# Performance work log

Measured on AMD Instinct MI355X. Metric: run time of the kernel, lower is better.

## Reference

```python
import jax, jax.numpy as jnp
import numpy as np

B, T = 256, 25
PRE = 2048   # resnet feature dim
D = 256      # fc_early_dim = cell_size = in_size = hybrid_in_size
K = 4        # num_atts
NC = 2       # num_classes


def setup_inputs() -> dict:
    key = jax.random.key(0)
    ks = jax.random.split(key, 20)
    def p(k, *s):
        return jax.random.normal(k, s, jnp.float32) * 0.02
    z = lambda *s: jnp.zeros(s, jnp.float32)
    return {
        "x_visual": jax.random.normal(ks[0], (B, T, PRE), jnp.float32),
        "x_tactile": jax.random.normal(ks[1], (B, T, PRE), jnp.float32),
        "fc0_w": p(ks[2], PRE, D), "fc0_b": z(D),
        "fc1_w": p(ks[3], PRE, D), "fc1_b": z(D),
        # LSTHM_V: W(x) + U(h) + V(z), gates packed as [f,i,o,ch]
        "lv_W": p(ks[4], D, 4 * D), "lv_U": p(ks[5], D, 4 * D), "lv_V": p(ks[6], D, 4 * D), "lv_b": z(4 * D),
        # LSTHM_T
        "lt_W": p(ks[7], D, 4 * D), "lt_U": p(ks[8], D, 4 * D), "lt_V": p(ks[9], D, 4 * D), "lt_b": z(4 * D),
        # MAB: attention over concat hidden (2D) producing K attentions
        "att_w": p(ks[10], 2 * D, K * 2 * D), "att_b": z(K * 2 * D),
        "red_v_w": p(ks[11], K * D, D), "red_v_b": z(D),
        "red_t_w": p(ks[12], K * D, D), "red_t_b": z(D),
        "mab_out_w": p(ks[13], 2 * D, D), "mab_out_b": z(D),
        "late0_w": p(ks[14], 2 * D, D), "late0_b": z(D),
        "late1_w": p(ks[15], D, NC), "late1_b": z(NC),
    }


def _lsthm(x, c, h, zz, W, U, V, b):
    s = x @ W + h @ U + zz @ V + b            # [B, 4D]
    f = jax.nn.sigmoid(s[:, :D])
    i = jax.nn.sigmoid(s[:, D:2 * D])
    o = jax.nn.sigmoid(s[:, 2 * D:3 * D])
    ch = jnp.tanh(s[:, 3 * D:])
    c_new = f * c + i * ch
    return c_new, jnp.tanh(c_new) * o


def reference(x_visual, x_tactile, fc0_w, fc0_b, fc1_w, fc1_b,
              lv_W, lv_U, lv_V, lv_b, lt_W, lt_U, lt_V, lt_b,
              att_w, att_b, red_v_w, red_v_b, red_t_w, red_t_b,
              mab_out_w, mab_out_b, late0_w, late0_b, late1_w, late1_b):
    xv = x_visual @ fc0_w + fc0_b             # [B, T, D]
    xt = x_tactile @ fc1_w + fc1_b            # [B, T, D]

    def mab(h_v, h_t):
        h = jnp.concatenate([h_v, h_t], -1)   # [B, 2D]
        att = jax.nn.softmax(h @ att_w + att_b, axis=-1)       # [B, K*2D]
        attd = att.reshape(-1, K, 2 * D) * h[:, None, :]        # K attended copies
        v = attd[:, :, :D].reshape(-1, K * D)
        t = attd[:, :, D:].reshape(-1, K * D)
        rv = jax.nn.relu(v @ red_v_w + red_v_b)
        rt = jax.nn.relu(t @ red_t_w + red_t_b)
        return jnp.concatenate([rv, rt], -1) @ mab_out_w + mab_out_b  # [B, D]

    def step(carry, xs):
        c_v, h_v, c_t, h_t, zz = carry
        xvi, xti = xs
        c_v, h_v = _lsthm(xvi, c_v, h_v, zz, lv_W, lv_U, lv_V, lv_b)
        c_t, h_t = _lsthm(xti, c_t, h_t, zz, lt_W, lt_U, lt_V, lt_b)
        zz = mab(h_v, h_t)
        return (c_v, h_v, c_t, h_t, zz), None

    zeros = jnp.zeros((x_visual.shape[0], D), jnp.float32)
    init = (zeros, zeros, zeros, zeros, zeros)
    (c_v, h_v, c_t, h_t, zz), _ = jax.lax.scan(
        step, init, (jnp.swapaxes(xv, 0, 1), jnp.swapaxes(xt, 0, 1)))
    x = jnp.concatenate([h_v, h_t], -1) @ late0_w + late0_b
    return x @ late1_w + late1_b              # dropout is identity in eval
```

## Files before the change

### kernel.cpp

```cpp
#include <hip/hip_runtime.h>

typedef unsigned short u16;
typedef unsigned int u32;
typedef unsigned long long u64;
using bfrag = __attribute__((ext_vector_type(8))) short;
using facc  = __attribute__((ext_vector_type(4))) float;

#define DEV __device__ __forceinline__
#define AGT __HIP_MEMORY_SCOPE_AGENT

static constexpr size_t o_xv  = 0;
static constexpr size_t o_xt  = 3276800;
static constexpr size_t o_Wxv = 6553600;
static constexpr size_t o_Wxt = 19660800;
static constexpr size_t o_f0T = 32768000;
static constexpr size_t o_f1T = 33816576;
static constexpr size_t o_UV  = 34865152;
static constexpr size_t o_Wpv = 36962304;
static constexpr size_t o_Wpt = 37486592;
static constexpr size_t o_bpv = 38010880;
static constexpr size_t o_bpt = 38014976;
static constexpr size_t o_attT= 38019072;
static constexpr size_t o_redT= 40116224;
static constexpr size_t o_mabT= 41164800;
static constexpr size_t o_FW  = 41426944;
static constexpr size_t o_fb  = 41431040;
static constexpr size_t o_eh  = 41431296;
static constexpr size_t o_rvt = 42479872;
static constexpr size_t o_ps  = 42742016;
static constexpr size_t o_hv0 = 42807552;
static constexpr size_t o_hv1 = 42938624;
static constexpr size_t o_ht0 = 43069696;
static constexpr size_t o_ht1 = 43200768;
static constexpr size_t o_zz  = 43331840;
static constexpr size_t o_bar = 43462912;
static constexpr size_t o_end = 43463936;

DEV u16 f2bf(float f) {
    u32 u = __float_as_uint(f);
    u32 r = (u + 0x7FFFu + ((u >> 16) & 1u)) >> 16;
    return (u16)r;
}
DEV float bf2f(u16 h) { return __uint_as_float(((u32)h) << 16); }
DEV u32 pk2(float a, float b) { return (u32)f2bf(a) | ((u32)f2bf(b) << 16); }
DEV float sigm(float x) { return 1.0f / (1.0f + __expf(-x)); }
DEV float tanh2(float x) { return 2.0f * sigm(2.0f * x) - 1.0f; }
DEV facc mfma16(bfrag a, bfrag b, facc c) {
    return __builtin_amdgcn_mfma_f32_16x16x32_bf16(a, b, c, 0, 0, 0);
}

DEV u64 ld64c(const void* p) { return __hip_atomic_load((u64*)p, __ATOMIC_RELAXED, AGT); }
DEV uint4 ld_c16(const void* p) {
    u64 a = ld64c(p), b = ld64c((const char*)p + 8);
    uint4 r; r.x = (u32)a; r.y = (u32)(a >> 32); r.z = (u32)b; r.w = (u32)(b >> 32); return r;
}
DEV float ldf32c(const float* p) {
    return __uint_as_float(__hip_atomic_load((u32*)p, __ATOMIC_RELAXED, AGT));
}
DEV void sw32(void* p, u32 v) { (void)__hip_atomic_exchange((u32*)p, v, __ATOMIC_RELAXED, AGT); }
DEV void sw64(void* p, u64 v) { (void)__hip_atomic_exchange((u64*)p, v, __ATOMIC_RELAXED, AGT); }
DEV void sw128(void* p, uint4 v) {
    sw64(p, ((u64)v.y << 32) | v.x);
    sw64((char*)p + 8, ((u64)v.w << 32) | v.z);
}
DEV void swf32(float* p, float v) { sw32(p, __float_as_uint(v)); }

DEV void gbar(u32* bar, int bid, u32 k) {
    asm volatile("s_waitcnt vmcnt(0)" ::: "memory");
    __syncthreads();
    if (threadIdx.x == 0) {
        __builtin_amdgcn_fence(__ATOMIC_RELEASE, "agent");
        u32 old = __hip_atomic_fetch_add(&bar[(bid & 7) * 16], 1u, __ATOMIC_RELAXED, AGT);
        if (old == k * 32u - 1u)
            __hip_atomic_fetch_add(&bar[128], 1u, __ATOMIC_RELAXED, AGT);
        while (__hip_atomic_load(&bar[128], __ATOMIC_RELAXED, AGT) < k * 8u)
            __builtin_amdgcn_s_sleep(2);
    }
    __syncthreads();
}


DEV void prep_T(const float* __restrict__ src, u16* dst, int lgK, int N, int nb, int bl, int tid) {
    int pairs = ((1 << lgK) * N) >> 1;
    int kmask = (1 << lgK) - 1;
    for (int idx = bl * 256 + tid; idx < pairs; idx += nb * 256) {
        int i = idx * 2;
        int n = i >> lgK, k = i & kmask;
        sw32(dst + i, pk2(src[(size_t)k * N + n], src[(size_t)(k + 1) * N + n]));
    }
}

DEV void prep_UV(const float* U, const float* V, u16* dst, int nb, int bl, int tid) {
    for (int idx = bl * 256 + tid; idx < 262144; idx += nb * 256) {
        int i = idx * 2;
        int p = i >> 9, k = i & 511;
        int j = p >> 2, g = p & 3;
        float v0 = (k < 256) ? U[(size_t)k * 1024 + g * 256 + j] : V[(size_t)(k - 256) * 1024 + g * 256 + j];
        float v1 = (k + 1 < 256) ? U[(size_t)(k + 1) * 1024 + g * 256 + j] : V[(size_t)(k - 255) * 1024 + g * 256 + j];
        sw32(dst + i, pk2(v0, v1));
    }
}

DEV void prep_W(const float* W, const float* bsrc, u16* dst, float* bpk, int nb, int bl, int tid) {
    for (int idx = bl * 256 + tid; idx < 131072; idx += nb * 256) {
        int i = idx * 2;
        int p = i >> 8, k = i & 255;
        int j = p >> 2, g = p & 3;
        sw32(dst + i, pk2(W[(size_t)k * 1024 + g * 256 + j], W[(size_t)(k + 1) * 1024 + g * 256 + j]));
        if (k == 0) swf32(&bpk[p], bsrc[g * 256 + j]);
    }
}

DEV void prep_FW(const float* l0w, const float* l0b, const float* l1w, const float* l1b,
                 float* FW, float* fb, int tid) {
    for (int idx = tid; idx < 1024; idx += 256) {
        int k = idx >> 1, c = idx & 1;
        float a = 0.f;
        for (int j = 0; j < 256; ++j) a += l0w[k * 256 + j] * l1w[j * 2 + c];
        swf32(&FW[idx], a);
    }
    if (tid < 2) {
        float a = l1b[tid];
        for (int j = 0; j < 256; ++j) a += l0b[j] * l1w[j * 2 + tid];
        swf32(&fb[tid], a);
    }
}

struct KP { const float* in[26]; char* ws; float* out; };


__global__ __launch_bounds__(256) void marn_all(KP P) {
    __shared__ __align__(16) unsigned char SM[31744];
    int tid = threadIdx.x, b = blockIdx.x;
    int w = tid >> 6, l = tid & 63, lm = l & 15, kh = l >> 4;
    u32 bk = 0;
    char* ws = P.ws;

    u16* f0T = (u16*)(ws + o_f0T);
    u16* f1T = (u16*)(ws + o_f1T);
    u16* attT = (u16*)(ws + o_attT);
    u16* redT = (u16*)(ws + o_redT);
    u16* mabT = (u16*)(ws + o_mabT);
    u16* UVpk = (u16*)(ws + o_UV);
    u16* Wpv = (u16*)(ws + o_Wpv);
    u16* Wpt = (u16*)(ws + o_Wpt);
    float* bpv = (float*)(ws + o_bpv);
    float* bpt = (float*)(ws + o_bpt);
    float* FW = (float*)(ws + o_FW);
    float* fb = (float*)(ws + o_fb);
    u16* xv = (u16*)(ws + o_xv);
    u16* xt = (u16*)(ws + o_xt);
    u16* Wxv = (u16*)(ws + o_Wxv);
    u16* Wxt = (u16*)(ws + o_Wxt);
    u16* eh = (u16*)(ws + o_eh);
    u16* rvt = (u16*)(ws + o_rvt);
    u16* hv0 = (u16*)(ws + o_hv0);
    u16* hv1 = (u16*)(ws + o_hv1);
    u16* ht0 = (u16*)(ws + o_ht0);
    u16* ht1 = (u16*)(ws + o_ht1);
    u16* zz = (u16*)(ws + o_zz);
    float* psum = (float*)(ws + o_ps);
    u32* bar = (u32*)(ws + o_bar);
    const float* attb = P.in[15];
    const float* rvb = P.in[17];
    const float* rtb = P.in[19];
    const float* mob = P.in[21];

    if      (b < 32)  prep_T(P.in[2], f0T, 11, 256, 32, b, tid);
    else if (b < 64)  prep_T(P.in[4], f1T, 11, 256, 32, b - 32, tid);
    else if (b < 128) prep_T(P.in[14], attT, 9, 2048, 64, b - 64, tid);
    else if (b < 144) prep_T(P.in[16], redT, 10, 256, 16, b - 128, tid);
    else if (b < 160) prep_T(P.in[18], redT + 256 * 1024, 10, 256, 16, b - 144, tid);
    else if (b < 168) prep_T(P.in[20], mabT, 9, 256, 8, b - 160, tid);
    else if (b < 200) prep_UV(P.in[7], P.in[8], UVpk, 32, b - 168, tid);
    else if (b < 232) prep_UV(P.in[11], P.in[12], UVpk + 1024 * 512, 32, b - 200, tid);
    else if (b < 244) prep_W(P.in[6], P.in[9], Wpv, bpv, 12, b - 232, tid);
    else if (b < 255) prep_W(P.in[10], P.in[13], Wpt, bpt, 11, b - 244, tid);
    else              prep_FW(P.in[22], P.in[23], P.in[24], P.in[25], FW, fb, tid);
    gbar(bar, b, ++bk);

    {
        u16* Al = (u16*)SM;
        u16* Bl = (u16*)(SM + 9216);
        u16* Lt = (u16*)SM;
        for (int u = b; u < 400; u += 256) {
            int zs = u & 1, ny = (u >> 1) & 1, mx = u >> 2;
            const float* A = zs ? P.in[1] : P.in[0];
            const u16* BT = zs ? f1T : f0T;
            const float* bias = zs ? P.in[5] : P.in[3];
            u16* C = zs ? xt : xv;
            int m0 = mx * 64, n0 = ny * 128;
            int arow = tid >> 2, aseg = tid & 3;
            int brow = tid >> 1, bseg = tid & 1;
            facc acc[8];
#pragma unroll
            for (int i = 0; i < 8; ++i) acc[i] = (facc){0.f, 0.f, 0.f, 0.f};
            for (int c = 0; c < 32; ++c) {
                float4 av[4];
#pragma unroll
                for (int uu = 0; uu < 4; ++uu)
                    av[uu] = *(const float4*)&A[(size_t)(m0 + arow) * 2048 + c * 64 + aseg * 16 + uu * 4];
                uint4 bv[4];
#pragma unroll
                for (int uu = 0; uu < 4; ++uu)
                    bv[uu] = *(const uint4*)&BT[(size_t)(n0 + brow) * 2048 + c * 64 + bseg * 32 + uu * 8];
                __syncthreads();
                u32 pk[8];
#pragma unroll
                for (int uu = 0; uu < 4; ++uu) {
                    pk[2 * uu] = pk2(av[uu].x, av[uu].y);
                    pk[2 * uu + 1] = pk2(av[uu].z, av[uu].w);
                }
                *(uint4*)&Al[arow * 72 + aseg * 16] = make_uint4(pk[0], pk[1], pk[2], pk[3]);
                *(uint4*)&Al[arow * 72 + aseg * 16 + 8] = make_uint4(pk[4], pk[5], pk[6], pk[7]);
#pragma unroll
                for (int uu = 0; uu < 4; ++uu)
                    *(uint4*)&Bl[brow * 72 + bseg * 32 + uu * 8] = bv[uu];
                __syncthreads();
#pragma unroll
                for (int ks = 0; ks < 2; ++ks) {
                    bfrag a = *(const bfrag*)&Al[(16 * w + lm) * 72 + ks * 32 + kh * 8];
#pragma unroll
                    for (int tt = 0; tt < 8; ++tt) {
                        bfrag bb = *(const bfrag*)&Bl[(tt * 16 + lm) * 72 + ks * 32 + kh * 8];
                        acc[tt] = mfma16(a, bb, acc[tt]);
                    }
                }
            }
            __syncthreads();
#pragma unroll
            for (int tt = 0; tt < 8; ++tt)
#pragma unroll
                for (int j = 0; j < 4; ++j)
                    Lt[(16 * w + 4 * kh + j) * 128 + tt * 16 + lm] = f2bf(acc[tt][j] + bias[n0 + tt * 16 + lm]);
            __syncthreads();
            {
                int mloc = tid >> 2, seg = tid & 3;
                const uint4* lp = (const uint4*)&Lt[mloc * 128 + seg * 32];
                sw128(&C[(size_t)(m0 + mloc) * 256 + n0 + seg * 32], lp[0]);
                sw128(&C[(size_t)(m0 + mloc) * 256 + n0 + seg * 32 + 8], lp[1]);
                sw128(&C[(size_t)(m0 + mloc) * 256 + n0 + seg * 32 + 16], lp[2]);
                sw128(&C[(size_t)(m0 + mloc) * 256 + n0 + seg * 32 + 24], lp[3]);
            }
            __syncthreads();
        }
    }
    gbar(bar, b, ++bk);

    {
        u16* Al = (u16*)SM;
        u16* Bl = (u16*)(SM + 9216);
        u16* Lt = (u16*)SM;
        for (int u = b; u < 1600; u += 256) {
            int mx = u >> 4, rem = u & 15;
            int ny = rem >> 1, zs = rem & 1;
            const u16* A = zs ? xt : xv;
            const u16* BT = zs ? Wpt : Wpv;
            const float* bpk = zs ? bpt : bpv;
            u16* O = zs ? Wxt : Wxv;
            int m0 = mx * 64, n0 = ny * 128;
            int arow = tid >> 2, aseg = tid & 3;
            int brow = tid >> 1, bseg = tid & 1;
            facc acc[8];
#pragma unroll
            for (int i = 0; i < 8; ++i) acc[i] = (facc){0.f, 0.f, 0.f, 0.f};
            for (int c = 0; c < 4; ++c) {
                uint4 av[2];
#pragma unroll
                for (int uu = 0; uu < 2; ++uu)
                    av[uu] = *(const uint4*)&A[(size_t)(m0 + arow) * 256 + c * 64 + aseg * 16 + uu * 8];
                uint4 bv[4];
#pragma unroll
                for (int uu = 0; uu < 4; ++uu)
                    bv[uu] = *(const uint4*)&BT[(size_t)(n0 + brow) * 256 + c * 64 + bseg * 32 + uu * 8];
                __syncthreads();
#pragma unroll
                for (int uu = 0; uu < 2; ++uu)
                    *(uint4*)&Al[arow * 72 + aseg * 16 + uu * 8] = av[uu];
#pragma unroll
                for (int uu = 0; uu < 4; ++uu)
                    *(uint4*)&Bl[brow * 72 + bseg * 32 + uu * 8] = bv[uu];
                __syncthreads();
#pragma unroll
                for (int ks = 0; ks < 2; ++ks) {
                    bfrag a = *(const bfrag*)&Al[(16 * w + lm) * 72 + ks * 32 + kh * 8];
#pragma unroll
                    for (int tt = 0; tt < 8; ++tt) {
                        bfrag bb = *(const bfrag*)&Bl[(tt * 16 + lm) * 72 + ks * 32 + kh * 8];
                        acc[tt] = mfma16(a, bb, acc[tt]);
                    }
                }
            }
            __syncthreads();
#pragma unroll
            for (int tt = 0; tt < 8; ++tt)
#pragma unroll
                for (int j = 0; j < 4; ++j)
                    Lt[(16 * w + 4 * kh + j) * 128 + tt * 16 + lm] = f2bf(acc[tt][j] + bpk[n0 + tt * 16 + lm]);
            __syncthreads();
            {
                int mloc = tid >> 2, seg = tid & 3;
                int mg = m0 + mloc;
                int bi = mg / 25, ti = mg - bi * 25;
                const uint4* lp = (const uint4*)&Lt[mloc * 128 + seg * 32];
                sw128(&O[(size_t)(ti * 256 + bi) * 1024 + n0 + seg * 32], lp[0]);
                sw128(&O[(size_t)(ti * 256 + bi) * 1024 + n0 + seg * 32 + 8], lp[1]);
                sw128(&O[(size_t)(ti * 256 + bi) * 1024 + n0 + seg * 32 + 16], lp[2]);
                sw128(&O[(size_t)(ti * 256 + bi) * 1024 + n0 + seg * 32 + 24], lp[3]);
            }
            __syncthreads();
        }
    }
    gbar(bar, b, ++bk);

    u16* Al = (u16*)SM;
    u16* Bl = (u16*)(SM + 17408);
    float* sscr = (float*)SM;
    float* ppart = (float*)(SM + 26112);
    float* sinvl = (float*)(SM + 27136);
    float* redscr = (float*)(SM + 27200);
    float creg[2] = {0.f, 0.f};

    for (int t = 0; t < 25; ++t) {
        const u16* hvp = (t & 1) ? hv1 : hv0;
        const u16* htp = (t & 1) ? ht1 : ht0;
        u16* hvc = (t & 1) ? hv0 : hv1;
        u16* htc = (t & 1) ? ht0 : ht1;

        {
            int m = b >> 6, n = b & 63;
            int r0 = m * 64, p0 = n * 32;
            bool sv = (n < 32);
            const u16* hsrc = sv ? hvp : htp;
            int arow = tid >> 2, aseg = tid & 3;
            int brow = tid >> 3, bseg = tid & 7;
            uint4 ar[2][4], br[2][2];
#pragma unroll
            for (int u = 0; u < 4; ++u)
                ar[0][u] = ld_c16(&hsrc[(r0 + arow) * 256 + aseg * 32 + u * 8]);
#pragma unroll
            for (int u = 0; u < 2; ++u)
                br[0][u] = *(const uint4*)&UVpk[(p0 + brow) * 512 + bseg * 16 + u * 8];
            facc acc0 = (facc){0.f, 0.f, 0.f, 0.f}, acc1 = (facc){0.f, 0.f, 0.f, 0.f};
#pragma unroll
            for (int c = 0; c < 4; ++c) {
                int cb = c & 1;
                __syncthreads();
#pragma unroll
                for (int u = 0; u < 4; ++u)
                    *(uint4*)&Al[arow * 136 + aseg * 32 + u * 8] = ar[cb][u];
#pragma unroll
                for (int u = 0; u < 2; ++u)
                    *(uint4*)&Bl[brow * 136 + bseg * 16 + u * 8] = br[cb][u];
                __syncthreads();
                if (c < 3) {
                    int cn = c + 1, nb = cb ^ 1;
                    const u16* asrc = (cn < 2) ? hsrc : zz;
                    int koff = (cn & 1) * 128;
#pragma unroll
                    for (int u = 0; u < 4; ++u)
                        ar[nb][u] = ld_c16(&asrc[(r0 + arow) * 256 + koff + aseg * 32 + u * 8]);
#pragma unroll
                    for (int u = 0; u < 2; ++u)
                        br[nb][u] = *(const uint4*)&UVpk[(p0 + brow) * 512 + cn * 128 + bseg * 16 + u * 8];
                }
#pragma unroll
                for (int ks = 0; ks < 4; ++ks) {
                    bfrag a = *(const bfrag*)&Al[(16 * w + lm) * 136 + ks * 32 + kh * 8];
                    bfrag b0 = *(const bfrag*)&Bl[lm * 136 + ks * 32 + kh * 8];
                    bfrag b1 = *(const bfrag*)&Bl[(16 + lm) * 136 + ks * 32 + kh * 8];
                    acc0 = mfma16(a, b0, acc0);
                    acc1 = mfma16(a, b1, acc1);
                }
            }
            __syncthreads();
#pragma unroll
            for (int j = 0; j < 4; ++j) {
                sscr[(16 * w + 4 * kh + j) * 33 + lm] = acc0[j];
                sscr[(16 * w + 4 * kh + j) * 33 + 16 + lm] = acc1[j];
            }
            __syncthreads();
            const u16* wxs = sv ? Wxv : Wxt;
            u16* hw = sv ? hvc : htc;
            int pl0 = sv ? p0 : (p0 - 1024);
            int r = tid >> 2, jp = tid & 3;
            uint4 wx4 = *(const uint4*)&wxs[(size_t)(t * 256 + r0 + r) * 1024 + pl0 + jp * 8];
            const u16* wxp = (const u16*)&wx4;
            float h2[2];
#pragma unroll
            for (int e = 0; e < 2; ++e) {
                int p = jp * 8 + e * 4;
                float s0 = sscr[r * 33 + p + 0] + bf2f(wxp[e * 4 + 0]);
                float s1 = sscr[r * 33 + p + 1] + bf2f(wxp[e * 4 + 1]);
                float s2 = sscr[r * 33 + p + 2] + bf2f(wxp[e * 4 + 2]);
                float s3 = sscr[r * 33 + p + 3] + bf2f(wxp[e * 4 + 3]);
                float fg = sigm(s0), ig = sigm(s1), og = sigm(s2), ch = tanh2(s3);
                float cn = fg * creg[e] + ig * ch;
                creg[e] = cn;
                h2[e] = tanh2(cn) * og;
            }
            sw32(&hw[(r0 + r) * 256 + (pl0 >> 2) + jp * 2], pk2(h2[0], h2[1]));
        }
        gbar(bar, b, ++bk);

        if (t < 24) {
            {
                int m = b >> 6, n = b & 63;
                int r0 = m * 64, c0 = n * 32;
                int arow = tid >> 2, aseg = tid & 3;
                int brow = tid >> 3, bseg = tid & 7;
                uint4 ar[2][4], br[2][2];
#pragma unroll
                for (int u = 0; u < 4; ++u)
                    ar[0][u] = ld_c16(&hvc[(r0 + arow) * 256 + aseg * 32 + u * 8]);
#pragma unroll
                for (int u = 0; u < 2; ++u)
                    br[0][u] = *(const uint4*)&attT[(c0 + brow) * 512 + bseg * 16 + u * 8];
                facc acc0 = (facc){0.f, 0.f, 0.f, 0.f}, acc1 = (facc){0.f, 0.f, 0.f, 0.f};
#pragma unroll
                for (int c = 0; c < 4; ++c) {
                    int cb = c & 1;
                    __syncthreads();
#pragma unroll
                    for (int u = 0; u < 4; ++u)
                        *(uint4*)&Al[arow * 136 + aseg * 32 + u * 8] = ar[cb][u];
#pragma unroll
                    for (int u = 0; u < 2; ++u)
                        *(uint4*)&Bl[brow * 136 + bseg * 16 + u * 8] = br[cb][u];
                    __syncthreads();
                    if (c < 3) {
                        int cn = c + 1, nb = cb ^ 1;
                        const u16* asrc = (cn < 2) ? hvc : htc;
                        int koff = (cn & 1) * 128;
#pragma unroll
                        for (int u = 0; u < 4; ++u)
                            ar[nb][u] = ld_c16(&asrc[(r0 + arow) * 256 + koff + aseg * 32 + u * 8]);
#pragma unroll
                        for (int u = 0; u < 2; ++u)
                            br[nb][u] = *(const uint4*)&attT[(c0 + brow) * 512 + cn * 128 + bseg * 16 + u * 8];
                    }
#pragma unroll
                    for (int ks = 0; ks < 4; ++ks) {
                        bfrag a = *(const bfrag*)&Al[(16 * w + lm) * 136 + ks * 32 + kh * 8];
                        bfrag b0 = *(const bfrag*)&Bl[lm * 136 + ks * 32 + kh * 8];
                        bfrag b1 = *(const bfrag*)&Bl[(16 + lm) * 136 + ks * 32 + kh * 8];
                        acc0 = mfma16(a, b0, acc0);
                        acc1 = mfma16(a, b1, acc1);
                    }
                }
                __syncthreads();
#pragma unroll
                for (int j = 0; j < 4; ++j) {
                    sscr[(16 * w + 4 * kh + j) * 33 + lm] = acc0[j];
                    sscr[(16 * w + 4 * kh + j) * 33 + 16 + lm] = acc1[j];
                }
                __syncthreads();
                int r = tid >> 2, q = tid & 3;
                int n15 = n & 15;
                const u16* hfs = (n15 < 8) ? hvc : htc;
                int hc0 = (32 * n15) & 255;
                uint4 hfv = ld_c16(&hfs[(r0 + r) * 256 + hc0 + q * 8]);
                const u16* hfp = (const u16*)&hfv;
                float ps = 0.f;
                u32 pk[4];
#pragma unroll
                for (int x = 0; x < 4; ++x) {
                    float e0 = __expf(sscr[r * 33 + q * 8 + 2 * x] + attb[c0 + q * 8 + 2 * x]);
                    float e1 = __expf(sscr[r * 33 + q * 8 + 2 * x + 1] + attb[c0 + q * 8 + 2 * x + 1]);
                    ps += e0 + e1;
                    pk[x] = (u32)f2bf(e0 * bf2f(hfp[2 * x])) | ((u32)f2bf(e1 * bf2f(hfp[2 * x + 1])) << 16);
                }
                sw64(&eh[(size_t)(r0 + r) * 2048 + c0 + q * 8], ((u64)pk[1] << 32) | pk[0]);
                sw64(&eh[(size_t)(r0 + r) * 2048 + c0 + q * 8 + 4], ((u64)pk[3] << 32) | pk[2]);
                ppart[r * 4 + q] = ps;
                __syncthreads();
                if (tid < 64) {
                    float s = ppart[tid * 4] + ppart[tid * 4 + 1] + ppart[tid * 4 + 2] + ppart[tid * 4 + 3];
                    swf32(&psum[n * 256 + r0 + tid], s);
                }
            }
            gbar(bar, b, ++bk);

            {
                int m = b >> 4, n = b & 15;
                int r0 = m * 16, nc0 = n * 32;
                int half = (n < 8) ? 0 : 1;
                if (tid < 64) {
                    int r = tid >> 2, q = tid & 3;
                    float s = 0.f;
                    for (int j2 = q * 16; j2 < q * 16 + 16; ++j2) s += ldf32c(&psum[j2 * 256 + r0 + r]);
                    ppart[r * 4 + q] = s;
                }
                __syncthreads();
                if (tid < 16)
                    sinvl[tid] = 1.0f / (ppart[tid * 4] + ppart[tid * 4 + 1] + ppart[tid * 4 + 2] + ppart[tid * 4 + 3]);
                int arow = tid >> 4, aseg = tid & 15;
                int brow = tid >> 3, bseg = tid & 7;
                uint4 ar[2], br[2][2];
                ar[0] = ld_c16(&eh[(size_t)(r0 + arow) * 2048 + half * 256 + aseg * 8]);
#pragma unroll
                for (int u = 0; u < 2; ++u)
                    br[0][u] = *(const uint4*)&redT[(nc0 + brow) * 1024 + bseg * 16 + u * 8];
                int tt = w & 1, kh2 = w >> 1;
                facc acc = (facc){0.f, 0.f, 0.f, 0.f};
#pragma unroll
                for (int c = 0; c < 8; ++c) {
                    int cb = c & 1;
                    __syncthreads();
                    *(uint4*)&Al[arow * 136 + aseg * 8] = ar[cb];
#pragma unroll
                    for (int u = 0; u < 2; ++u)
                        *(uint4*)&Bl[brow * 136 + bseg * 16 + u * 8] = br[cb][u];
                    __syncthreads();
                    if (c < 7) {
                        int cn = c + 1, nb = cb ^ 1;
                        ar[nb] = ld_c16(&eh[(size_t)(r0 + arow) * 2048 + (cn >> 1) * 512 + half * 256 + (cn & 1) * 128 + aseg * 8]);
#pragma unroll
                        for (int u = 0; u < 2; ++u)
                            br[nb][u] = *(const uint4*)&redT[(nc0 + brow) * 1024 + cn * 128 + bseg * 16 + u * 8];
                    }
#pragma unroll
                    for (int k2 = 0; k2 < 2; ++k2) {
                        int ks = kh2 * 2 + k2;
                        bfrag a = *(const bfrag*)&Al[lm * 136 + ks * 32 + kh * 8];
                        bfrag bb = *(const bfrag*)&Bl[(tt * 16 + lm) * 136 + ks * 32 + kh * 8];
                        acc = mfma16(a, bb, acc);
                    }
                }
                __syncthreads();
                if (w >= 2) {
#pragma unroll
                    for (int j = 0; j < 4; ++j)
                        redscr[tt * 272 + (4 * kh + j) * 17 + lm] = acc[j];
                }
                __syncthreads();
                if (w < 2) {
#pragma unroll
                    for (int j = 0; j < 4; ++j) {
                        float v = acc[j] + redscr[tt * 272 + (4 * kh + j) * 17 + lm];
                        int rloc = 4 * kh + j;
                        int col = nc0 + tt * 16 + lm;
                        float bs = (col < 256) ? rvb[col] : rtb[col - 256];
                        v = fmaxf(sinvl[rloc] * v + bs, 0.0f);
                        sscr[rloc * 33 + tt * 16 + lm] = v;
                    }
                }
                __syncthreads();
                {
                    int rloc = tid >> 4, cp = tid & 15;
                    sw32(&rvt[(r0 + rloc) * 512 + nc0 + 2 * cp],
                         pk2(sscr[rloc * 33 + 2 * cp], sscr[rloc * 33 + 2 * cp + 1]));
                }
            }
            gbar(bar, b, ++bk);

            {
                int m = b >> 4, n = b & 15;
                int r0 = m * 16, nc0 = n * 16;
                int arow = tid >> 4, aseg = tid & 15;
                uint4 ar[2], br[2];
                ar[0] = ld_c16(&rvt[(r0 + arow) * 512 + aseg * 8]);
                br[0] = *(const uint4*)&mabT[(nc0 + arow) * 512 + aseg * 8];
                facc acc = (facc){0.f, 0.f, 0.f, 0.f};
#pragma unroll
                for (int c = 0; c < 4; ++c) {
                    int cb = c & 1;
                    __syncthreads();
                    *(uint4*)&Al[arow * 136 + aseg * 8] = ar[cb];
                    *(uint4*)&Bl[arow * 136 + aseg * 8] = br[cb];
                    __syncthreads();
                    if (c < 3) {
                        ar[cb ^ 1] = ld_c16(&rvt[(r0 + arow) * 512 + (c + 1) * 128 + aseg * 8]);
                        br[cb ^ 1] = *(const uint4*)&mabT[(nc0 + arow) * 512 + (c + 1) * 128 + aseg * 8];
                    }
                    bfrag a = *(const bfrag*)&Al[lm * 136 + w * 32 + kh * 8];
                    bfrag bb = *(const bfrag*)&Bl[lm * 136 + w * 32 + kh * 8];
                    acc = mfma16(a, bb, acc);
                }
                __syncthreads();
                if (w > 0) {
#pragma unroll
                    for (int j = 0; j < 4; ++j)
                        redscr[(w - 1) * 272 + (4 * kh + j) * 17 + lm] = acc[j];
                }
                __syncthreads();
                if (w == 0) {
#pragma unroll
                    for (int j = 0; j < 4; ++j) {
                        int idx = (4 * kh + j) * 17 + lm;
                        float v = acc[j] + redscr[idx] + redscr[272 + idx] + redscr[544 + idx] + mob[nc0 + lm];
                        sscr[(4 * kh + j) * 33 + lm] = v;
                    }
                }
                __syncthreads();
                if (tid < 128) {
                    int rloc = tid >> 3, cp = tid & 7;
                    sw32(&zz[(r0 + rloc) * 256 + nc0 + 2 * cp],
                         pk2(sscr[rloc * 33 + 2 * cp], sscr[rloc * 33 + 2 * cp + 1]));
                }
            }
            gbar(bar, b, ++bk);
        }
    }

    {
        if (tid < 64) {
            float a0 = 0.f, a1 = 0.f;
            u64 hv = ld64c(&hv1[b * 256 + tid * 4]);
            u64 ht = ld64c(&ht1[b * 256 + tid * 4]);
#pragma unroll
            for (int i = 0; i < 4; ++i) {
                int k = tid * 4 + i;
                float h0 = bf2f((u16)(hv >> (16 * i)));
                float h1 = bf2f((u16)(ht >> (16 * i)));
                a0 += h0 * FW[k * 2] + h1 * FW[(256 + k) * 2];
                a1 += h0 * FW[k * 2 + 1] + h1 * FW[(256 + k) * 2 + 1];
            }
            ppart[tid] = a0;
            ppart[64 + tid] = a1;
        }
        __syncthreads();
        if (tid < 2) {
            float s = ldf32c(&fb[tid]);
            for (int i = 0; i < 64; ++i) s += ppart[tid * 64 + i];
            P.out[b * 2 + tid] = s;
        }
    }
}


extern "C" void kernel_launch(void* const* d_in, const int* in_sizes, int n_in,
                              void* d_out, int out_size, void* d_ws, size_t ws_size,
                              hipStream_t stream) {
    (void)in_sizes; (void)n_in; (void)out_size; (void)ws_size;
    KP P;
    for (int i = 0; i < 26; ++i) P.in[i] = (const float*)d_in[i];
    P.ws = (char*)d_ws;
    P.out = (float*)d_out;

    hipMemsetAsync((char*)d_ws + o_hv0, 0, o_end - o_hv0, stream);

    void* kargs[] = { &P };
    hipError_t e = hipLaunchCooperativeKernel((void*)marn_all, dim3(256), dim3(256),
                                              kargs, 0, stream);
    if (e != hipSuccess) {
        (void)hipGetLastError();
        marn_all<<<dim3(256), dim3(256), 0, stream>>>(P);
    }
}
```

Measured before the change: 1.749 ms.

## Fold MAB output projection into gate weights and drop per-step mab stage

Precomputes mab_out_w·V per LSTHM so the recurrent gate GEMM consumes the reduced [rv,rt] vector directly, with x-projection concatenated as a combined [U|moV|W] K=1024 weight. This removes the separate x@W pre-GEMM phase and one grid barrier per timestep (the mab_out GEMM). Per-timestep buffers for h, eh, psum and rvt replace ping-pong buffers, so atomic coherent loads/stores become plain ones. Loads go straight from global into MFMA fragments without LDS staging. The risks are the larger per-step K and uncached plain loads on data written by other blocks, plus a more expensive O(256^3) prep product done in-kernel.

```diff
diff --git a/kernel.cpp b/kernel.cpp
--- a/kernel.cpp
+++ b/kernel.cpp
@@ -9,32 +9,27 @@
 #define DEV __device__ __forceinline__
 #define AGT __HIP_MEMORY_SCOPE_AGENT
 
-static constexpr size_t o_xv  = 0;
-static constexpr size_t o_xt  = 3276800;
-static constexpr size_t o_Wxv = 6553600;
-static constexpr size_t o_Wxt = 19660800;
-static constexpr size_t o_f0T = 32768000;
-static constexpr size_t o_f1T = 33816576;
-static constexpr size_t o_UV  = 34865152;
-static constexpr size_t o_Wpv = 36962304;
-static constexpr size_t o_Wpt = 37486592;
-static constexpr size_t o_bpv = 38010880;
-static constexpr size_t o_bpt = 38014976;
-static constexpr size_t o_attT= 38019072;
-static constexpr size_t o_redT= 40116224;
-static constexpr size_t o_mabT= 41164800;
-static constexpr size_t o_FW  = 41426944;
-static constexpr size_t o_fb  = 41431040;
-static constexpr size_t o_eh  = 41431296;
-static constexpr size_t o_rvt = 42479872;
-static constexpr size_t o_ps  = 42742016;
-static constexpr size_t o_hv0 = 42807552;
-static constexpr size_t o_hv1 = 42938624;
-static constexpr size_t o_ht0 = 43069696;
-static constexpr size_t o_ht1 = 43200768;
-static constexpr size_t o_zz  = 43331840;
-static constexpr size_t o_bar = 43462912;
-static constexpr size_t o_end = 43463936;
+static constexpr size_t o_xv   = 0;
+static constexpr size_t o_xt   = 3276800;
+static constexpr size_t o_f0T  = 6553600;
+static constexpr size_t o_f1T  = 7602176;
+static constexpr size_t o_UVWv = 8650752;
+static constexpr size_t o_UVWt = 10747904;
+static constexpr size_t o_attT = 12845056;
+static constexpr size_t o_redT = 14942208;
+static constexpr size_t o_bgv  = 15990784;
+static constexpr size_t o_bgt  = 15994880;
+static constexpr size_t o_mvv  = 15998976;
+static constexpr size_t o_mvt  = 16003072;
+static constexpr size_t o_FW   = 16007168;
+static constexpr size_t o_fb   = 16011264;
+static constexpr size_t o_eh   = 16011520;
+static constexpr size_t o_psum = 41177344;
+static constexpr size_t o_hv   = 42750208;
+static constexpr size_t o_ht   = 46158080;
+static constexpr size_t o_rvt  = 49565952;
+static constexpr size_t o_bar  = 56119552;
+static constexpr size_t o_end  = 56120576;
 
 DEV u16 f2bf(float f) {
     u32 u = __float_as_uint(f);
@@ -48,22 +43,6 @@
 DEV facc mfma16(bfrag a, bfrag b, facc c) {
     return __builtin_amdgcn_mfma_f32_16x16x32_bf16(a, b, c, 0, 0, 0);
 }
-
-DEV u64 ld64c(const void* p) { return __hip_atomic_load((u64*)p, __ATOMIC_RELAXED, AGT); }
-DEV uint4 ld_c16(const void* p) {
-    u64 a = ld64c(p), b = ld64c((const char*)p + 8);
-    uint4 r; r.x = (u32)a; r.y = (u32)(a >> 32); r.z = (u32)b; r.w = (u32)(b >> 32); return r;
-}
-DEV float ldf32c(const float* p) {
-    return __uint_as_float(__hip_atomic_load((u32*)p, __ATOMIC_RELAXED, AGT));
-}
-DEV void sw32(void* p, u32 v) { (void)__hip_atomic_exchange((u32*)p, v, __ATOMIC_RELAXED, AGT); }
-DEV void sw64(void* p, u64 v) { (void)__hip_atomic_exchange((u64*)p, v, __ATOMIC_RELAXED, AGT); }
-DEV void sw128(void* p, uint4 v) {
-    sw64(p, ((u64)v.y << 32) | v.x);
-    sw64((char*)p + 8, ((u64)v.w << 32) | v.z);
-}
-DEV void swf32(float* p, float v) { sw32(p, __float_as_uint(v)); }
 
 DEV void gbar(u32* bar, int bid, u32 k) {
     asm volatile("s_waitcnt vmcnt(0)" ::: "memory");
@@ -86,28 +65,35 @@
     for (int idx = bl * 256 + tid; idx < pairs; idx += nb * 256) {
         int i = idx * 2;
         int n = i >> lgK, k = i & kmask;
-        sw32(dst + i, pk2(src[(size_t)k * N + n], src[(size_t)(k + 1) * N + n]));
-    }
-}
-
-DEV void prep_UV(const float* U, const float* V, u16* dst, int nb, int bl, int tid) {
-    for (int idx = bl * 256 + tid; idx < 262144; idx += nb * 256) {
-        int i = idx * 2;
-        int p = i >> 9, k = i & 511;
-        int j = p >> 2, g = p & 3;
-        float v0 = (k < 256) ? U[(size_t)k * 1024 + g * 256 + j] : V[(size_t)(k - 256) * 1024 + g * 256 + j];
-        float v1 = (k + 1 < 256) ? U[(size_t)(k + 1) * 1024 + g * 256 + j] : V[(size_t)(k - 255) * 1024 + g * 256 + j];
-        sw32(dst + i, pk2(v0, v1));
-    }
-}
-
-DEV void prep_W(const float* W, const float* bsrc, u16* dst, float* bpk, int nb, int bl, int tid) {
-    for (int idx = bl * 256 + tid; idx < 131072; idx += nb * 256) {
-        int i = idx * 2;
-        int p = i >> 8, k = i & 255;
-        int j = p >> 2, g = p & 3;
-        sw32(dst + i, pk2(W[(size_t)k * 1024 + g * 256 + j], W[(size_t)(k + 1) * 1024 + g * 256 + j]));
-        if (k == 0) swf32(&bpk[p], bsrc[g * 256 + j]);
+        *(u32*)&dst[i] = pk2(src[(size_t)k * N + n], src[(size_t)(k + 1) * N + n]);
+    }
+}
+
+DEV void prep_UVW(const float* U, const float* mo, const float* V, const float* W,
+                  u16* dst, int nb, int bl, int tid) {
+    for (int idx = bl * 256 + tid; idx < 1024 * 1024; idx += nb * 256) {
+        int p = idx >> 10, k = idx & 1023;
+        int j = p >> 2, g = p & 3, gc = g * 256 + j;
+        float v;
+        if (k < 256) v = U[(size_t)k * 1024 + gc];
+        else if (k < 768) {
+            int s = k - 256;
+            float a = 0.f;
+            for (int d = 0; d < 256; ++d) a += mo[s * 256 + d] * V[(size_t)d * 1024 + gc];
+            v = a;
+        } else v = W[(size_t)(k - 768) * 1024 + gc];
+        dst[idx] = f2bf(v);
+    }
+}
+
+DEV void prep_bias(const float* lb, const float* mob, const float* V,
+                   float* bg, float* mv, int nb, int bl, int tid) {
+    for (int p = bl * 256 + tid; p < 1024; p += nb * 256) {
+        int j = p >> 2, g = p & 3, gc = g * 256 + j;
+        bg[p] = lb[gc];
+        float a = 0.f;
+        for (int d = 0; d < 256; ++d) a += mob[d] * V[(size_t)d * 1024 + gc];
+        mv[p] = a;
     }
 }
 
@@ -117,17 +103,16 @@
         int k = idx >> 1, c = idx & 1;
         float a = 0.f;
         for (int j = 0; j < 256; ++j) a += l0w[k * 256 + j] * l1w[j * 2 + c];
-        swf32(&FW[idx], a);
+        FW[idx] = a;
     }
     if (tid < 2) {
         float a = l1b[tid];
         for (int j = 0; j < 256; ++j) a += l0b[j] * l1w[j * 2 + tid];
-        swf32(&fb[tid], a);
+        fb[tid] = a;
     }
 }
 
 struct KP { const float* in[26]; char* ws; float* out; };
-
 
 __global__ __launch_bounds__(256) void marn_all(KP P) {
     __shared__ __align__(16) unsigned char SM[31744];
@@ -136,47 +121,40 @@
     u32 bk = 0;
     char* ws = P.ws;
 
+    u16* xv = (u16*)(ws + o_xv);
+    u16* xt = (u16*)(ws + o_xt);
     u16* f0T = (u16*)(ws + o_f0T);
     u16* f1T = (u16*)(ws + o_f1T);
+    u16* UVWv = (u16*)(ws + o_UVWv);
+    u16* UVWt = (u16*)(ws + o_UVWt);
     u16* attT = (u16*)(ws + o_attT);
     u16* redT = (u16*)(ws + o_redT);
-    u16* mabT = (u16*)(ws + o_mabT);
-    u16* UVpk = (u16*)(ws + o_UV);
-    u16* Wpv = (u16*)(ws + o_Wpv);
-    u16* Wpt = (u16*)(ws + o_Wpt);
-    float* bpv = (float*)(ws + o_bpv);
-    float* bpt = (float*)(ws + o_bpt);
+    float* bgv = (float*)(ws + o_bgv);
+    float* bgt = (float*)(ws + o_bgt);
+    float* mvv = (float*)(ws + o_mvv);
+    float* mvt = (float*)(ws + o_mvt);
     float* FW = (float*)(ws + o_FW);
     float* fb = (float*)(ws + o_fb);
-    u16* xv = (u16*)(ws + o_xv);
-    u16* xt = (u16*)(ws + o_xt);
-    u16* Wxv = (u16*)(ws + o_Wxv);
-    u16* Wxt = (u16*)(ws + o_Wxt);
-    u16* eh = (u16*)(ws + o_eh);
-    u16* rvt = (u16*)(ws + o_rvt);
-    u16* hv0 = (u16*)(ws + o_hv0);
-    u16* hv1 = (u16*)(ws + o_hv1);
-    u16* ht0 = (u16*)(ws + o_ht0);
-    u16* ht1 = (u16*)(ws + o_ht1);
-    u16* zz = (u16*)(ws + o_zz);
-    float* psum = (float*)(ws + o_ps);
+    u16* ehB = (u16*)(ws + o_eh);
+    float* psB = (float*)(ws + o_psum);
+    u16* hvB = (u16*)(ws + o_hv);
+    u16* htB = (u16*)(ws + o_ht);
+    u16* rvB = (u16*)(ws + o_rvt);
     u32* bar = (u32*)(ws + o_bar);
     const float* attb = P.in[15];
     const float* rvb = P.in[17];
     const float* rtb = P.in[19];
-    const float* mob = P.in[21];
-
-    if      (b < 32)  prep_T(P.in[2], f0T, 11, 256, 32, b, tid);
-    else if (b < 64)  prep_T(P.in[4], f1T, 11, 256, 32, b - 32, tid);
-    else if (b < 128) prep_T(P.in[14], attT, 9, 2048, 64, b - 64, tid);
-    else if (b < 144) prep_T(P.in[16], redT, 10, 256, 16, b - 128, tid);
-    else if (b < 160) prep_T(P.in[18], redT + 256 * 1024, 10, 256, 16, b - 144, tid);
-    else if (b < 168) prep_T(P.in[20], mabT, 9, 256, 8, b - 160, tid);
-    else if (b < 200) prep_UV(P.in[7], P.in[8], UVpk, 32, b - 168, tid);
-    else if (b < 232) prep_UV(P.in[11], P.in[12], UVpk + 1024 * 512, 32, b - 200, tid);
-    else if (b < 244) prep_W(P.in[6], P.in[9], Wpv, bpv, 12, b - 232, tid);
-    else if (b < 255) prep_W(P.in[10], P.in[13], Wpt, bpt, 11, b - 244, tid);
-    else              prep_FW(P.in[22], P.in[23], P.in[24], P.in[25], FW, fb, tid);
+
+    if      (b < 24)  prep_T(P.in[2], f0T, 11, 256, 24, b, tid);
+    else if (b < 48)  prep_T(P.in[4], f1T, 11, 256, 24, b - 24, tid);
+    else if (b < 96)  prep_T(P.in[14], attT, 9, 2048, 48, b - 48, tid);
+    else if (b < 108) prep_T(P.in[16], redT, 10, 256, 12, b - 96, tid);
+    else if (b < 120) prep_T(P.in[18], redT + 256 * 1024, 10, 256, 12, b - 108, tid);
+    else if (b < 176) prep_UVW(P.in[7], P.in[20], P.in[8], P.in[6], UVWv, 56, b - 120, tid);
+    else if (b < 232) prep_UVW(P.in[11], P.in[20], P.in[12], P.in[10], UVWt, 56, b - 176, tid);
+    else if (b < 236) prep_bias(P.in[9], P.in[21], P.in[8], bgv, mvv, 4, b - 232, tid);
+    else if (b < 240) prep_bias(P.in[13], P.in[21], P.in[12], bgt, mvt, 4, b - 236, tid);
+    else if (b == 240) prep_FW(P.in[22], P.in[23], P.in[24], P.in[25], FW, fb, tid);
     gbar(bar, b, ++bk);
 
     {
@@ -236,85 +214,19 @@
             __syncthreads();
             {
                 int mloc = tid >> 2, seg = tid & 3;
+                int mg = m0 + mloc;
+                int bi = mg / 25, ti = mg - bi * 25;
+                u16* drow = &C[(size_t)(ti * 256 + bi) * 256 + n0 + seg * 32];
                 const uint4* lp = (const uint4*)&Lt[mloc * 128 + seg * 32];
-                sw128(&C[(size_t)(m0 + mloc) * 256 + n0 + seg * 32], lp[0]);
-                sw128(&C[(size_t)(m0 + mloc) * 256 + n0 + seg * 32 + 8], lp[1]);
-                sw128(&C[(size_t)(m0 + mloc) * 256 + n0 + seg * 32 + 16], lp[2]);
-                sw128(&C[(size_t)(m0 + mloc) * 256 + n0 + seg * 32 + 24], lp[3]);
+#pragma unroll
+                for (int i = 0; i < 4; ++i)
+                    *(uint4*)&drow[i * 8] = lp[i];
             }
             __syncthreads();
         }
     }
     gbar(bar, b, ++bk);
 
-    {
-        u16* Al = (u16*)SM;
-        u16* Bl = (u16*)(SM + 9216);
-        u16* Lt = (u16*)SM;
-        for (int u = b; u < 1600; u += 256) {
-            int mx = u >> 4, rem = u & 15;
-            int ny = rem >> 1, zs = rem & 1;
-            const u16* A = zs ? xt : xv;
-            const u16* BT = zs ? Wpt : Wpv;
-            const float* bpk = zs ? bpt : bpv;
-            u16* O = zs ? Wxt : Wxv;
-            int m0 = mx * 64, n0 = ny * 128;
-            int arow = tid >> 2, aseg = tid & 3;
-            int brow = tid >> 1, bseg = tid & 1;
-            facc acc[8];
-#pragma unroll
-            for (int i = 0; i < 8; ++i) acc[i] = (facc){0.f, 0.f, 0.f, 0.f};
-            for (int c = 0; c < 4; ++c) {
-                uint4 av[2];
-#pragma unroll
-                for (int uu = 0; uu < 2; ++uu)
-                    av[uu] = *(const uint4*)&A[(size_t)(m0 + arow) * 256 + c * 64 + aseg * 16 + uu * 8];
-                uint4 bv[4];
-#pragma unroll
-                for (int uu = 0; uu < 4; ++uu)
-                    bv[uu] = *(const uint4*)&BT[(size_t)(n0 + brow) * 256 + c * 64 + bseg * 32 + uu * 8];
-                __syncthreads();
-#pragma unroll
-                for (int uu = 0; uu < 2; ++uu)
-                    *(uint4*)&Al[arow * 72 + aseg * 16 + uu * 8] = av[uu];
-#pragma unroll
-                for (int uu = 0; uu < 4; ++uu)
-                    *(uint4*)&Bl[brow * 72 + bseg * 32 + uu * 8] = bv[uu];
-                __syncthreads();
-#pragma unroll
-                for (int ks = 0; ks < 2; ++ks) {
-                    bfrag a = *(const bfrag*)&Al[(16 * w + lm) * 72 + ks * 32 + kh * 8];
-#pragma unroll
-                    for (int tt = 0; tt < 8; ++tt) {
-                        bfrag bb = *(const bfrag*)&Bl[(tt * 16 + lm) * 72 + ks * 32 + kh * 8];
-                        acc[tt] = mfma16(a, bb, acc[tt]);
-                    }
-                }
-            }
-            __syncthreads();
-#pragma unroll
-            for (int tt = 0; tt < 8; ++tt)
-#pragma unroll
-                for (int j = 0; j < 4; ++j)
-                    Lt[(16 * w + 4 * kh + j) * 128 + tt * 16 + lm] = f2bf(acc[tt][j] + bpk[n0 + tt * 16 + lm]);
-            __syncthreads();
-            {
-                int mloc = tid >> 2, seg = tid & 3;
-                int mg = m0 + mloc;
-                int bi = mg / 25, ti = mg - bi * 25;
-                const uint4* lp = (const uint4*)&Lt[mloc * 128 + seg * 32];
-                sw128(&O[(size_t)(ti * 256 + bi) * 1024 + n0 + seg * 32], lp[0]);
-                sw128(&O[(size_t)(ti * 256 + bi) * 1024 + n0 + seg * 32 + 8], lp[1]);
-                sw128(&O[(size_t)(ti * 256 + bi) * 1024 + n0 + seg * 32 + 16], lp[2]);
-                sw128(&O[(size_t)(ti * 256 + bi) * 1024 + n0 + seg * 32 + 24], lp[3]);
-            }
-            __syncthreads();
-        }
-    }
-    gbar(bar, b, ++bk);
-
-    u16* Al = (u16*)SM;
-    u16* Bl = (u16*)(SM + 17408);
     float* sscr = (float*)SM;
     float* ppart = (float*)(SM + 26112);
     float* sinvl = (float*)(SM + 27136);
@@ -322,56 +234,50 @@
     float creg[2] = {0.f, 0.f};
 
     for (int t = 0; t < 25; ++t) {
-        const u16* hvp = (t & 1) ? hv1 : hv0;
-        const u16* htp = (t & 1) ? ht1 : ht0;
-        u16* hvc = (t & 1) ? hv0 : hv1;
-        u16* htc = (t & 1) ? ht0 : ht1;
+        const u16* hv_t = hvB + t * 65536;
+        const u16* ht_t = htB + t * 65536;
+        u16* hv_n = hvB + (t + 1) * 65536;
+        u16* ht_n = htB + (t + 1) * 65536;
+        const u16* rv_t = rvB + t * 131072;
 
         {
-            int m = b >> 6, n = b & 63;
-            int r0 = m * 64, p0 = n * 32;
+            int m = b & 3, n = b >> 2;
+            int r0 = m * 64;
             bool sv = (n < 32);
-            const u16* hsrc = sv ? hvp : htp;
-            int arow = tid >> 2, aseg = tid & 3;
-            int brow = tid >> 3, bseg = tid & 7;
-            uint4 ar[2][4], br[2][2];
-#pragma unroll
-            for (int u = 0; u < 4; ++u)
-                ar[0][u] = ld_c16(&hsrc[(r0 + arow) * 256 + aseg * 32 + u * 8]);
-#pragma unroll
-            for (int u = 0; u < 2; ++u)
-                br[0][u] = *(const uint4*)&UVpk[(p0 + brow) * 512 + bseg * 16 + u * 8];
+            int p0 = (sv ? n : n - 32) * 32;
+            const u16* UVW = sv ? UVWv : UVWt;
+            const u16* hb = sv ? hv_t : ht_t;
+            const u16* xb = (sv ? xv : xt) + t * 65536;
+            int arow = r0 + 16 * w + lm;
+            const u16* Ah = hb + arow * 256 + kh * 8;
+            const u16* Ar = rv_t + arow * 512 + kh * 8;
+            const u16* Ax = xb + arow * 256 + kh * 8;
+            const u16* B0 = UVW + (size_t)(p0 + lm) * 1024 + kh * 8;
+            const u16* B1 = UVW + (size_t)(p0 + 16 + lm) * 1024 + kh * 8;
             facc acc0 = (facc){0.f, 0.f, 0.f, 0.f}, acc1 = (facc){0.f, 0.f, 0.f, 0.f};
 #pragma unroll
-            for (int c = 0; c < 4; ++c) {
-                int cb = c & 1;
-                __syncthreads();
-#pragma unroll
-                for (int u = 0; u < 4; ++u)
-                    *(uint4*)&Al[arow * 136 + aseg * 32 + u * 8] = ar[cb][u];
-#pragma unroll
-                for (int u = 0; u < 2; ++u)
-                    *(uint4*)&Bl[brow * 136 + bseg * 16 + u * 8] = br[cb][u];
-                __syncthreads();
-                if (c < 3) {
-                    int cn = c + 1, nb = cb ^ 1;
-                    const u16* asrc = (cn < 2) ? hsrc : zz;
-                    int koff = (cn & 1) * 128;
-#pragma unroll
-                    for (int u = 0; u < 4; ++u)
-                        ar[nb][u] = ld_c16(&asrc[(r0 + arow) * 256 + koff + aseg * 32 + u * 8]);
-#pragma unroll
-                    for (int u = 0; u < 2; ++u)
-                        br[nb][u] = *(const uint4*)&UVpk[(p0 + brow) * 512 + cn * 128 + bseg * 16 + u * 8];
-                }
-#pragma unroll
-                for (int ks = 0; ks < 4; ++ks) {
-                    bfrag a = *(const bfrag*)&Al[(16 * w + lm) * 136 + ks * 32 + kh * 8];
-                    bfrag b0 = *(const bfrag*)&Bl[lm * 136 + ks * 32 + kh * 8];
-                    bfrag b1 = *(const bfrag*)&Bl[(16 + lm) * 136 + ks * 32 + kh * 8];
-                    acc0 = mfma16(a, b0, acc0);
-                    acc1 = mfma16(a, b1, acc1);
-                }
+            for (int ks = 0; ks < 8; ++ks) {
+                bfrag a = *(const bfrag*)(Ah + ks * 32);
+                bfrag b0 = *(const bfrag*)(B0 + ks * 32);
+                bfrag b1 = *(const bfrag*)(B1 + ks * 32);
+                acc0 = mfma16(a, b0, acc0);
+                acc1 = mfma16(a, b1, acc1);
+            }
+#pragma unroll
+            for (int ks = 0; ks < 16; ++ks) {
+                bfrag a = *(const bfrag*)(Ar + ks * 32);
+                bfrag b0 = *(const bfrag*)(B0 + 256 + ks * 32);
+                bfrag b1 = *(const bfrag*)(B1 + 256 + ks * 32);
+                acc0 = mfma16(a, b0, acc0);
+                acc1 = mfma16(a, b1, acc1);
+            }
+#pragma unroll
+            for (int ks = 0; ks < 8; ++ks) {
+                bfrag a = *(const bfrag*)(Ax + ks * 32);
+                bfrag b0 = *(const bfrag*)(B0 + 768 + ks * 32);
+                bfrag b1 = *(const bfrag*)(B1 + 768 + ks * 32);
+                acc0 = mfma16(a, b0, acc0);
+                acc1 = mfma16(a, b1, acc1);
             }
             __syncthreads();
 #pragma unroll
@@ -380,73 +286,58 @@
                 sscr[(16 * w + 4 * kh + j) * 33 + 16 + lm] = acc1[j];
             }
             __syncthreads();
-            const u16* wxs = sv ? Wxv : Wxt;
-            u16* hw = sv ? hvc : htc;
-            int pl0 = sv ? p0 : (p0 - 1024);
+            const float* bg = sv ? bgv : bgt;
+            const float* mv = sv ? mvv : mvt;
+            float tf = (t > 0) ? 1.0f : 0.0f;
             int r = tid >> 2, jp = tid & 3;
-            uint4 wx4 = *(const uint4*)&wxs[(size_t)(t * 256 + r0 + r) * 1024 + pl0 + jp * 8];
-            const u16* wxp = (const u16*)&wx4;
             float h2[2];
 #pragma unroll
             for (int e = 0; e < 2; ++e) {
                 int p = jp * 8 + e * 4;
-                float s0 = sscr[r * 33 + p + 0] + bf2f(wxp[e * 4 + 0]);
-                float s1 = sscr[r * 33 + p + 1] + bf2f(wxp[e * 4 + 1]);
-                float s2 = sscr[r * 33 + p + 2] + bf2f(wxp[e * 4 + 2]);
-                float s3 = sscr[r * 33 + p + 3] + bf2f(wxp[e * 4 + 3]);
+                float4 b4 = *(const float4*)&bg[p0 + p];
+                float4 m4 = *(const float4*)&mv[p0 + p];
+                float s0 = sscr[r * 33 + p + 0] + b4.x + tf * m4.x;
+                float s1 = sscr[r * 33 + p + 1] + b4.y + tf * m4.y;
+                float s2 = sscr[r * 33 + p + 2] + b4.z + tf * m4.z;
+                float s3 = sscr[r * 33 + p + 3] + b4.w + tf * m4.w;
                 float fg = sigm(s0), ig = sigm(s1), og = sigm(s2), ch = tanh2(s3);
                 float cn = fg * creg[e] + ig * ch;
                 creg[e] = cn;
                 h2[e] = tanh2(cn) * og;
             }
-            sw32(&hw[(r0 + r) * 256 + (pl0 >> 2) + jp * 2], pk2(h2[0], h2[1]));
+            u16* hw = sv ? hv_n : ht_n;
+            *(u32*)&hw[(r0 + r) * 256 + (p0 >> 2) + jp * 2] = pk2(h2[0], h2[1]);
         }
         gbar(bar, b, ++bk);
 
         if (t < 24) {
+            u16* eh_t = ehB + (size_t)t * 524288;
+            float* ps_t = psB + t * 16384;
+
             {
-                int m = b >> 6, n = b & 63;
+                int m = b & 3, n = b >> 2;
                 int r0 = m * 64, c0 = n * 32;
-                int arow = tid >> 2, aseg = tid & 3;
-                int brow = tid >> 3, bseg = tid & 7;
-                uint4 ar[2][4], br[2][2];
-#pragma unroll
-                for (int u = 0; u < 4; ++u)
-                    ar[0][u] = ld_c16(&hvc[(r0 + arow) * 256 + aseg * 32 + u * 8]);
-#pragma unroll
-                for (int u = 0; u < 2; ++u)
-                    br[0][u] = *(const uint4*)&attT[(c0 + brow) * 512 + bseg * 16 + u * 8];
+                int arow = r0 + 16 * w + lm;
+                const u16* A0 = hv_n + arow * 256 + kh * 8;
+                const u16* A1 = ht_n + arow * 256 + kh * 8;
+                const u16* B0 = attT + (size_t)(c0 + lm) * 512 + kh * 8;
+                const u16* B1 = attT + (size_t)(c0 + 16 + lm) * 512 + kh * 8;
                 facc acc0 = (facc){0.f, 0.f, 0.f, 0.f}, acc1 = (facc){0.f, 0.f, 0.f, 0.f};
 #pragma unroll
-                for (int c = 0; c < 4; ++c) {
-                    int cb = c & 1;
-                    __syncthreads();
-#pragma unroll
-                    for (int u = 0; u < 4; ++u)
-                        *(uint4*)&Al[arow * 136 + aseg * 32 + u * 8] = ar[cb][u];
-#pragma unroll
-                    for (int u = 0; u < 2; ++u)
-                        *(uint4*)&Bl[brow * 136 + bseg * 16 + u * 8] = br[cb][u];
-                    __syncthreads();
-                    if (c < 3) {
-                        int cn = c + 1, nb = cb ^ 1;
-                        const u16* asrc = (cn < 2) ? hvc : htc;
-                        int koff = (cn & 1) * 128;
-#pragma unroll
-                        for (int u = 0; u < 4; ++u)
-                            ar[nb][u] = ld_c16(&asrc[(r0 + arow) * 256 + koff + aseg * 32 + u * 8]);
-#pragma unroll
-                        for (int u = 0; u < 2; ++u)
-                            br[nb][u] = *(const uint4*)&attT[(c0 + brow) * 512 + cn * 128 + bseg * 16 + u * 8];
-                    }
-#pragma unroll
-                    for (int ks = 0; ks < 4; ++ks) {
-                        bfrag a = *(const bfrag*)&Al[(16 * w + lm) * 136 + ks * 32 + kh * 8];
-                        bfrag b0 = *(const bfrag*)&Bl[lm * 136 + ks * 32 + kh * 8];
-                        bfrag b1 = *(const bfrag*)&Bl[(16 + lm) * 136 + ks * 32 + kh * 8];
-                        acc0 = mfma16(a, b0, acc0);
-                        acc1 = mfma16(a, b1, acc1);
-                    }
+                for (int ks = 0; ks < 8; ++ks) {
+                    bfrag a = *(const bfrag*)(A0 + ks * 32);
+                    bfrag b0 = *(const bfrag*)(B0 + ks * 32);
+                    bfrag b1 = *(const bfrag*)(B1 + ks * 32);
+                    acc0 = mfma16(a, b0, acc0);
+                    acc1 = mfma16(a, b1, acc1);
+                }
+#pragma unroll
+                for (int ks = 0; ks < 8; ++ks) {
+                    bfrag a = *(const bfrag*)(A1 + ks * 32);
+                    bfrag b0 = *(const bfrag*)(B0 + 256 + ks * 32);
+                    bfrag b1 = *(const bfrag*)(B1 + 256 + ks * 32);
+                    acc0 = mfma16(a, b0, acc0);
+                    acc1 = mfma16(a, b1, acc1);
                 }
                 __syncthreads();
 #pragma unroll
@@ -457,9 +348,9 @@
                 __syncthreads();
                 int r = tid >> 2, q = tid & 3;
                 int n15 = n & 15;
-                const u16* hfs = (n15 < 8) ? hvc : htc;
+                const u16* hfs = (n15 < 8) ? hv_n : ht_n;
                 int hc0 = (32 * n15) & 255;
-                uint4 hfv = ld_c16(&hfs[(r0 + r) * 256 + hc0 + q * 8]);
+                uint4 hfv = *(const uint4*)&hfs[(r0 + r) * 256 + hc0 + q * 8];
                 const u16* hfp = (const u16*)&hfv;
                 float ps = 0.f;
                 u32 pk[4];
@@ -470,62 +361,40 @@
                     ps += e0 + e1;
                     pk[x] = (u32)f2bf(e0 * bf2f(hfp[2 * x])) | ((u32)f2bf(e1 * bf2f(hfp[2 * x + 1])) << 16);
                 }
-                sw64(&eh[(size_t)(r0 + r) * 2048 + c0 + q * 8], ((u64)pk[1] << 32) | pk[0]);
-                sw64(&eh[(size_t)(r0 + r) * 2048 + c0 + q * 8 + 4], ((u64)pk[3] << 32) | pk[2]);
+                *(uint4*)&eh_t[(size_t)(r0 + r) * 2048 + c0 + q * 8] = make_uint4(pk[0], pk[1], pk[2], pk[3]);
                 ppart[r * 4 + q] = ps;
                 __syncthreads();
-                if (tid < 64) {
-                    float s = ppart[tid * 4] + ppart[tid * 4 + 1] + ppart[tid * 4 + 2] + ppart[tid * 4 + 3];
-                    swf32(&psum[n * 256 + r0 + tid], s);
-                }
+                if (tid < 64)
+                    ps_t[n * 256 + r0 + tid] =
+                        ppart[tid * 4] + ppart[tid * 4 + 1] + ppart[tid * 4 + 2] + ppart[tid * 4 + 3];
             }
             gbar(bar, b, ++bk);
 
             {
-                int m = b >> 4, n = b & 15;
+                int m = b & 15, n = b >> 4;
                 int r0 = m * 16, nc0 = n * 32;
                 int half = (n < 8) ? 0 : 1;
                 if (tid < 64) {
                     int r = tid >> 2, q = tid & 3;
                     float s = 0.f;
-                    for (int j2 = q * 16; j2 < q * 16 + 16; ++j2) s += ldf32c(&psum[j2 * 256 + r0 + r]);
+                    for (int j2 = q * 16; j2 < q * 16 + 16; ++j2) s += ps_t[j2 * 256 + r0 + r];
                     ppart[r * 4 + q] = s;
                 }
                 __syncthreads();
                 if (tid < 16)
                     sinvl[tid] = 1.0f / (ppart[tid * 4] + ppart[tid * 4 + 1] + ppart[tid * 4 + 2] + ppart[tid * 4 + 3]);
-                int arow = tid >> 4, aseg = tid & 15;
-                int brow = tid >> 3, bseg = tid & 7;
-                uint4 ar[2], br[2][2];
-                ar[0] = ld_c16(&eh[(size_t)(r0 + arow) * 2048 + half * 256 + aseg * 8]);
-#pragma unroll
-                for (int u = 0; u < 2; ++u)
-                    br[0][u] = *(const uint4*)&redT[(nc0 + brow) * 1024 + bseg * 16 + u * 8];
                 int tt = w & 1, kh2 = w >> 1;
+                const u16* Ab = eh_t + (size_t)(r0 + lm) * 2048 + half * 256 + kh * 8;
+                const u16* Bb = redT + (size_t)(nc0 + tt * 16 + lm) * 1024 + kh * 8;
                 facc acc = (facc){0.f, 0.f, 0.f, 0.f};
 #pragma unroll
-                for (int c = 0; c < 8; ++c) {
-                    int cb = c & 1;
-                    __syncthreads();
-                    *(uint4*)&Al[arow * 136 + aseg * 8] = ar[cb];
-#pragma unroll
-                    for (int u = 0; u < 2; ++u)
-                        *(uint4*)&Bl[brow * 136 + bseg * 16 + u * 8] = br[cb][u];
-                    __syncthreads();
-                    if (c < 7) {
-                        int cn = c + 1, nb = cb ^ 1;
-                        ar[nb] = ld_c16(&eh[(size_t)(r0 + arow) * 2048 + (cn >> 1) * 512 + half * 256 + (cn & 1) * 128 + aseg * 8]);
-#pragma unroll
-                        for (int u = 0; u < 2; ++u)
-                            br[nb][u] = *(const uint4*)&redT[(nc0 + brow) * 1024 + cn * 128 + bseg * 16 + u * 8];
-                    }
-#pragma unroll
-                    for (int k2 = 0; k2 < 2; ++k2) {
-                        int ks = kh2 * 2 + k2;
-                        bfrag a = *(const bfrag*)&Al[lm * 136 + ks * 32 + kh * 8];
-                        bfrag bb = *(const bfrag*)&Bl[(tt * 16 + lm) * 136 + ks * 32 + kh * 8];
-                        acc = mfma16(a, bb, acc);
-                    }
+                for (int s = 0; s < 16; ++s) {
+                    int ks = kh2 * 16 + s;
+                    int kk = ks * 32;
+                    int j = ((kk >> 8) << 9) + (kk & 255);
+                    bfrag a = *(const bfrag*)(Ab + j);
+                    bfrag bb = *(const bfrag*)(Bb + kk);
+                    acc = mfma16(a, bb, acc);
                 }
                 __syncthreads();
                 if (w >= 2) {
@@ -546,57 +415,14 @@
                     }
                 }
                 __syncthreads();
-                {
-                    int rloc = tid >> 4, cp = tid & 15;
-                    sw32(&rvt[(r0 + rloc) * 512 + nc0 + 2 * cp],
-                         pk2(sscr[rloc * 33 + 2 * cp], sscr[rloc * 33 + 2 * cp + 1]));
-                }
-            }
-            gbar(bar, b, ++bk);
-
-            {
-                int m = b >> 4, n = b & 15;
-                int r0 = m * 16, nc0 = n * 16;
-                int arow = tid >> 4, aseg = tid & 15;
-                uint4 ar[2], br[2];
-                ar[0] = ld_c16(&rvt[(r0 + arow) * 512 + aseg * 8]);
-                br[0] = *(const uint4*)&mabT[(nc0 + arow) * 512 + aseg * 8];
-                facc acc = (facc){0.f, 0.f, 0.f, 0.f};
-#pragma unroll
-                for (int c = 0; c < 4; ++c) {
-                    int cb = c & 1;
-                    __syncthreads();
-                    *(uint4*)&Al[arow * 136 + aseg * 8] = ar[cb];
-                    *(uint4*)&Bl[arow * 136 + aseg * 8] = br[cb];
-                    __syncthreads();
-                    if (c < 3) {
-                        ar[cb ^ 1] = ld_c16(&rvt[(r0 + arow) * 512 + (c + 1) * 128 + aseg * 8]);
-                        br[cb ^ 1] = *(const uint4*)&mabT[(nc0 + arow) * 512 + (c + 1) * 128 + aseg * 8];
-                    }
-                    bfrag a = *(const bfrag*)&Al[lm * 136 + w * 32 + kh * 8];
-                    bfrag bb = *(const bfrag*)&Bl[lm * 136 + w * 32 + kh * 8];
-                    acc = mfma16(a, bb, acc);
-                }
-                __syncthreads();
-                if (w > 0) {
-#pragma unroll
-                    for (int j = 0; j < 4; ++j)
-                        redscr[(w - 1) * 272 + (4 * kh + j) * 17 + lm] = acc[j];
-                }
-                __syncthreads();
-                if (w == 0) {
-#pragma unroll
-                    for (int j = 0; j < 4; ++j) {
-                        int idx = (4 * kh + j) * 17 + lm;
-                        float v = acc[j] + redscr[idx] + redscr[272 + idx] + redscr[544 + idx] + mob[nc0 + lm];
-                        sscr[(4 * kh + j) * 33 + lm] = v;
-                    }
-                }
-                __syncthreads();
-                if (tid < 128) {
-                    int rloc = tid >> 3, cp = tid & 7;
-                    sw32(&zz[(r0 + rloc) * 256 + nc0 + 2 * cp],
-                         pk2(sscr[rloc * 33 + 2 * cp], sscr[rloc * 33 + 2 * cp + 1]));
+                if (tid < 64) {
+                    int rloc = tid >> 2, cp = tid & 3;
+                    u16* rw = rvB + (size_t)(t + 1) * 131072;
+                    u32 q0 = pk2(sscr[rloc * 33 + cp * 8 + 0], sscr[rloc * 33 + cp * 8 + 1]);
+                    u32 q1 = pk2(sscr[rloc * 33 + cp * 8 + 2], sscr[rloc * 33 + cp * 8 + 3]);
+                    u32 q2 = pk2(sscr[rloc * 33 + cp * 8 + 4], sscr[rloc * 33 + cp * 8 + 5]);
+                    u32 q3 = pk2(sscr[rloc * 33 + cp * 8 + 6], sscr[rloc * 33 + cp * 8 + 7]);
+                    *(uint4*)&rw[(size_t)(r0 + rloc) * 512 + nc0 + cp * 8] = make_uint4(q0, q1, q2, q3);
                 }
             }
             gbar(bar, b, ++bk);
@@ -604,10 +430,12 @@
     }
 
     {
+        const u16* hv25 = hvB + 25 * 65536;
+        const u16* ht25 = htB + 25 * 65536;
         if (tid < 64) {
             float a0 = 0.f, a1 = 0.f;
-            u64 hv = ld64c(&hv1[b * 256 + tid * 4]);
-            u64 ht = ld64c(&ht1[b * 256 + tid * 4]);
+            u64 hv = *(const u64*)&hv25[b * 256 + tid * 4];
+            u64 ht = *(const u64*)&ht25[b * 256 + tid * 4];
 #pragma unroll
             for (int i = 0; i < 4; ++i) {
                 int k = tid * 4 + i;
@@ -621,7 +449,7 @@
         }
         __syncthreads();
         if (tid < 2) {
-            float s = ldf32c(&fb[tid]);
+            float s = fb[tid];
             for (int i = 0; i < 64; ++i) s += ppart[tid * 64 + i];
             P.out[b * 2 + tid] = s;
         }
@@ -638,7 +466,10 @@
     P.ws = (char*)d_ws;
     P.out = (float*)d_out;
 
-    hipMemsetAsync((char*)d_ws + o_hv0, 0, o_end - o_hv0, stream);
+    hipMemsetAsync((char*)d_ws + o_bar, 0, 1024, stream);
+    hipMemsetAsync((char*)d_ws + o_hv, 0, 131072, stream);
+    hipMemsetAsync((char*)d_ws + o_ht, 0, 131072, stream);
+    hipMemsetAsync((char*)d_ws + o_rvt, 0, 262144, stream);
 
     void* kargs[] = { &P };
     hipError_t e = hipLaunchCooperativeKernel((void*)marn_all, dim3(256), dim3(256),
```

Result: slower. 1.945 ms (+11.2%).
